# Kernel optimization log

Measured on AMD Instinct MI355X. Metric: run time of the kernel, lower is better.

## Reference

```python
import jax, jax.numpy as jnp
import numpy as np

NUM_EXPERTS = 8
TOP_K = 2
HIDDEN = 2048
FFN = 4096


def setup_inputs() -> dict:
    key = jax.random.key(0)
    ks = jax.random.split(key, 5)
    s = 0.02
    return {
        "hidden_states": jax.random.normal(ks[0], (2, 2048, HIDDEN), dtype=jnp.float32),
        "w_router": jax.random.normal(ks[1], (HIDDEN, NUM_EXPERTS), dtype=jnp.float32) * s,
        "w1": jax.random.normal(ks[2], (NUM_EXPERTS, FFN, HIDDEN), dtype=jnp.float32) * s,
        "w2": jax.random.normal(ks[3], (NUM_EXPERTS, HIDDEN, FFN), dtype=jnp.float32) * s,
        "w3": jax.random.normal(ks[4], (NUM_EXPERTS, FFN, HIDDEN), dtype=jnp.float32) * s,
    }


def reference(hidden_states, w_router, w1, w2, w3):
    shape = hidden_states.shape
    x = hidden_states.reshape(-1, HIDDEN)  # [T, H]

    # Router: logits -> softmax -> top-k -> renormalize (Mixtral routing)
    logits = x @ w_router                              # [T, E]
    probs = jax.nn.softmax(logits, axis=-1)
    top_w, top_i = jax.lax.top_k(probs, TOP_K)         # [T, K]
    top_w = top_w / jnp.sum(top_w, axis=-1, keepdims=True)
    # Dense combine weights per expert: [T, E]
    combine = jnp.sum(
        jax.nn.one_hot(top_i, NUM_EXPERTS, dtype=x.dtype) * top_w[..., None], axis=1
    )

    # Grouped SwiGLU experts: out = sum_e combine[:, e] * w2_e(silu(w1_e x) * w3_e x)
    out = jnp.zeros_like(x)
    for e in range(NUM_EXPERTS):
        h = jax.nn.silu(x @ w1[e].T) * (x @ w3[e].T)   # [T, F]
        y = h @ w2[e].T                                # [T, H]
        out = out + combine[:, e:e + 1] * y

    return (out.reshape(shape), jnp.zeros((1,), dtype=x.dtype))
```

## Files before the change

kernel.cpp:

```cpp
#include <hip/hip_runtime.h>
#include <hip/hip_bf16.h>
#include <stdint.h>

#define T_TOK 4096
#define HID   2048
#define FFN_D 4096
#define NE    8
#define PADB  256
#define PADMAX 10240

typedef __attribute__((ext_vector_type(8))) short  short8;
typedef __attribute__((ext_vector_type(4))) float  f32x4;
typedef __attribute__((ext_vector_type(4))) unsigned short u16x4;
typedef unsigned short u16;

__device__ __forceinline__ u16 f2bf(float f) {
    unsigned u = __float_as_uint(f);
    u += 0x7FFFu + ((u >> 16) & 1u);
    return (u16)(u >> 16);
}
__device__ __forceinline__ float bf2f(u16 v) {
    return __uint_as_float(((unsigned)v) << 16);
}

#define GLD16(g, l) __builtin_amdgcn_global_load_lds( \
    (const __attribute__((address_space(1))) unsigned int*)(g), \
    (__attribute__((address_space(3))) unsigned int*)(l), 16, 0, 0)

__global__ void k_convert(const float* __restrict__ s, u16* __restrict__ d, long n8) {
    for (long i = (long)blockIdx.x * 256 + threadIdx.x; i < n8; i += (long)gridDim.x * 256) {
        f32x4 a = *((const f32x4*)s + i * 2);
        f32x4 b = *((const f32x4*)s + i * 2 + 1);
        short8 o;
#pragma unroll
        for (int q = 0; q < 4; ++q) { o[q] = (short)f2bf(a[q]); o[q + 4] = (short)f2bf(b[q]); }
        *(short8*)(d + i * 8) = o;
    }
}

__global__ void k_router(const float* __restrict__ x, const float* __restrict__ wr,
                         int* __restrict__ topk_id, float* __restrict__ topk_w,
                         int* __restrict__ counts) {
    int lane = threadIdx.x & 63;
    int t = blockIdx.x * 4 + (threadIdx.x >> 6);
    const float* xr = x + (size_t)t * HID;
    float acc[8];
#pragma unroll
    for (int e = 0; e < 8; ++e) acc[e] = 0.f;
    for (int h = lane; h < HID; h += 64) {
        float xv = xr[h];
        f32x4 w0 = *(const f32x4*)(wr + h * 8);
        f32x4 w1 = *(const f32x4*)(wr + h * 8 + 4);
#pragma unroll
        for (int q = 0; q < 4; ++q) { acc[q] += xv * w0[q]; acc[4 + q] += xv * w1[q]; }
    }
#pragma unroll
    for (int e = 0; e < 8; ++e) {
        float v = acc[e];
#pragma unroll
        for (int s = 32; s > 0; s >>= 1) v += __shfl_xor(v, s);
        acc[e] = v;
    }
    if (lane == 0) {
        int i0 = 0; float l0 = acc[0];
#pragma unroll
        for (int e = 1; e < 8; ++e) if (acc[e] > l0) { l0 = acc[e]; i0 = e; }
        int i1 = -1; float l1 = -3.4e38f;
#pragma unroll
        for (int e = 0; e < 8; ++e) if (e != i0 && acc[e] > l1) { l1 = acc[e]; i1 = e; }
        float wA = 1.f / (1.f + expf(l1 - l0));
        topk_id[t * 2] = i0;  topk_id[t * 2 + 1] = i1;
        topk_w[t * 2] = wA;   topk_w[t * 2 + 1] = 1.f - wA;
        atomicAdd(&counts[i0], 1);
        atomicAdd(&counts[i1], 1);
    }
}

__global__ void k_scan(const int* __restrict__ counts, int* __restrict__ pad_off,
                       int* __restrict__ perm_tok) {
    __shared__ int sTot;
    if (threadIdx.x == 0) {
        int o = 0;
#pragma unroll
        for (int e = 0; e < 8; ++e) { pad_off[e] = o; o += ((counts[e] + PADB - 1) / PADB) * PADB; }
        pad_off[8] = o; sTot = o;
    }
    __syncthreads();
    int tot = sTot;
    for (int i = threadIdx.x; i < tot; i += 256) perm_tok[i] = 0;
}

__global__ void k_scatter(const int* __restrict__ topk_id, int* __restrict__ cursors,
                          const int* __restrict__ pad_off, int* __restrict__ perm_tok,
                          int* __restrict__ pos_of) {
    int t = blockIdx.x * 256 + threadIdx.x;
    if (t >= T_TOK) return;
#pragma unroll
    for (int k = 0; k < 2; ++k) {
        int e = topk_id[t * 2 + k];
        int p = pad_off[e] + atomicAdd(&cursors[e], 1);
        perm_tok[p] = t;
        pos_of[t * 2 + k] = p;
    }
}

template<int KTOT, int NTOT, int BNt, int KSPLIT, bool DUAL, bool GATHER>
__global__ __launch_bounds__(512, 2) void k_gemm8(
    const u16* __restrict__ A,
    const u16* __restrict__ B0all,
    const u16* __restrict__ B1all,
    u16* __restrict__ C,
    const int* __restrict__ perm_tok,
    const int* __restrict__ pad_off)
{
    constexpr int BMt   = 256;
    constexpr int WCW   = BNt / 4;
    constexpr int NI    = WCW / 16;
    constexpr int CPX   = (NTOT / BNt) / 8;
    constexpr int KPART = KTOT / KSPLIT;
    constexpr int NK    = KPART / 64;
    constexpr int ATILE = BMt * 64;
    constexpr int BTILE = BNt * 64;
    constexpr int SEGB  = DUAL ? 8 : (BNt == 256 ? 8 : 4);

    const int bid = blockIdx.x;
    const int xcd = bid & 7;
    int idx = bid >> 3;
    const int kh  = idx & (KSPLIT - 1);
    idx /= KSPLIT;
    const int m0  = (idx / CPX) * BMt;
    if (m0 >= pad_off[8]) return;
    const int n0  = (xcd * CPX + (idx % CPX)) * BNt;
    int e = 0;
    while (pad_off[e + 1] <= m0) ++e;

    __shared__ u16 As[2 * ATILE];
    __shared__ u16 Bs0[2 * BTILE];
    __shared__ u16 Bs1[DUAL ? 2 * BTILE : 8];
    __shared__ int tokS[GATHER ? BMt : 8];

    const int tid = threadIdx.x;
    const int w = tid >> 6, l = tid & 63;
    if (GATHER) {
        for (int i = tid; i < BMt; i += 512) tokS[i] = perm_tok[m0 + i];
        __syncthreads();
    }

    const u16* B0 = B0all + (size_t)e * NTOT * KTOT;
    const u16* B1 = DUAL ? (B1all + (size_t)e * NTOT * KTOT) : B0all;
    const int k0e = kh * KPART;

    const int nseg = (w < 4) ? 8 : SEGB;
    const u16* gsrc[8];
    u16* ldst[8];
    int tstep;
    {
        const int c = (l & 7) ^ (l >> 3);
#pragma unroll
        for (int j = 0; j < 8; ++j) {
            const int js = (j < nseg) ? j : (j - 4);
            const int rl = js * 8 + (l >> 3);
            if (w < 4) {
                const int rt = w * 64 + rl;
                const long grow = GATHER ? (long)tokS[rt] : (long)(m0 + rt);
                gsrc[j] = A + grow * KTOT + k0e + c * 8;
                ldst[j] = (u16*)As + (w * 64 + js * 8) * 64;
                tstep = ATILE;
            } else if (DUAL && w >= 6) {
                const int rt = (w - 6) * 64 + rl;
                gsrc[j] = B1 + (size_t)(n0 + rt) * KTOT + k0e + c * 8;
                ldst[j] = (u16*)Bs1 + (rt - rl + js * 8) * 64;
                tstep = BTILE;
            } else {
                const int rt = DUAL ? ((w - 4) * 64 + rl)
                                    : (BNt == 256 ? ((w - 4) * 64 + rl)
                                                  : ((w - 4) * 32 + rl));
                gsrc[j] = B0 + (size_t)(n0 + rt) * KTOT + k0e + c * 8;
                ldst[j] = (u16*)Bs0 + (rt - rl + js * 8) * 64;
                tstep = BTILE;
            }
        }
    }

    const int wr = w >> 2, wc = w & 3;
    const int fr = l & 15, fk = l >> 4, x7 = l & 7;
    const int pc0 = ((fk ^ x7) << 3);
    const int pc1 = pc0 ^ 32;
    const int aB = (wr * 128 + fr) * 64;
    const int bB = (wc * WCW + fr) * 64;

    f32x4 acc0[8][NI], acc1[8][NI];
    const f32x4 fz = {0.f, 0.f, 0.f, 0.f};
#pragma unroll
    for (int mi = 0; mi < 8; ++mi)
#pragma unroll
        for (int ni = 0; ni < NI; ++ni) { acc0[mi][ni] = fz; if (DUAL) acc1[mi][ni] = fz; }

#pragma unroll
    for (int j = 0; j < 8; ++j) if (j < nseg) GLD16(gsrc[j], ldst[j]);
    asm volatile("s_waitcnt vmcnt(0)" ::: "memory");
    __builtin_amdgcn_s_barrier();
    __builtin_amdgcn_sched_barrier(0);

#pragma unroll 1
    for (int t = 0; t < NK; ++t) {
        const int cb = t & 1, nb2 = cb ^ 1;
        const u16* aC  = (const u16*)As  + cb * ATILE;
        const u16* b0C = (const u16*)Bs0 + cb * BTILE;
        const u16* b1C = (const u16*)Bs1 + (DUAL ? cb * BTILE : 0);
        const long kE = (long)(t + 1) * 64;
        const bool hasNext = (t + 1 < NK);

        short8 af[4], b0f[NI], b1f[NI];

        if (hasNext) {
#pragma unroll
            for (int j = 0; j < 4; ++j) if (j < nseg) GLD16(gsrc[j] + kE, ldst[j] + nb2 * tstep);
        }
#pragma unroll
        for (int mi = 0; mi < 4; ++mi) af[mi] = *(const short8*)(aC + aB + mi * 1024 + pc0);
#pragma unroll
        for (int ni = 0; ni < NI; ++ni) {
            b0f[ni] = *(const short8*)(b0C + bB + ni * 1024 + pc0);
            if (DUAL) b1f[ni] = *(const short8*)(b1C + bB + ni * 1024 + pc0);
        }
        __builtin_amdgcn_s_setprio(1);
#pragma unroll
        for (int mi = 0; mi < 4; ++mi)
#pragma unroll
            for (int ni = 0; ni < NI; ++ni) {
                acc0[mi][ni] = __builtin_amdgcn_mfma_f32_16x16x32_bf16(af[mi], b0f[ni], acc0[mi][ni], 0, 0, 0);
                if (DUAL)
                    acc1[mi][ni] = __builtin_amdgcn_mfma_f32_16x16x32_bf16(af[mi], b1f[ni], acc1[mi][ni], 0, 0, 0);
            }
        __builtin_amdgcn_s_setprio(0);

        if (hasNext) {
#pragma unroll
            for (int j = 4; j < 8; ++j) if (j < nseg) GLD16(gsrc[j] + kE, ldst[j] + nb2 * tstep);
        }
#pragma unroll
        for (int mi = 0; mi < 4; ++mi) af[mi] = *(const short8*)(aC + aB + (mi + 4) * 1024 + pc0);
        __builtin_amdgcn_s_setprio(1);
#pragma unroll
        for (int mi = 0; mi < 4; ++mi)
#pragma unroll
            for (int ni = 0; ni < NI; ++ni) {
                acc0[mi + 4][ni] = __builtin_amdgcn_mfma_f32_16x16x32_bf16(af[mi], b0f[ni], acc0[mi + 4][ni], 0, 0, 0);
                if (DUAL)
                    acc1[mi + 4][ni] = __builtin_amdgcn_mfma_f32_16x16x32_bf16(af[mi], b1f[ni], acc1[mi + 4][ni], 0, 0, 0);
            }
        __builtin_amdgcn_s_setprio(0);

#pragma unroll
        for (int mi = 0; mi < 4; ++mi) af[mi] = *(const short8*)(aC + aB + mi * 1024 + pc1);
#pragma unroll
        for (int ni = 0; ni < NI; ++ni) {
            b0f[ni] = *(const short8*)(b0C + bB + ni * 1024 + pc1);
            if (DUAL) b1f[ni] = *(const short8*)(b1C + bB + ni * 1024 + pc1);
        }
        __builtin_amdgcn_s_setprio(1);
#pragma unroll
        for (int mi = 0; mi < 4; ++mi)
#pragma unroll
            for (int ni = 0; ni < NI; ++ni) {
                acc0[mi][ni] = __builtin_amdgcn_mfma_f32_16x16x32_bf16(af[mi], b0f[ni], acc0[mi][ni], 0, 0, 0);
                if (DUAL)
                    acc1[mi][ni] = __builtin_amdgcn_mfma_f32_16x16x32_bf16(af[mi], b1f[ni], acc1[mi][ni], 0, 0, 0);
            }
        __builtin_amdgcn_s_setprio(0);

#pragma unroll
        for (int mi = 0; mi < 4; ++mi) af[mi] = *(const short8*)(aC + aB + (mi + 4) * 1024 + pc1);
        __builtin_amdgcn_s_setprio(1);
#pragma unroll
        for (int mi = 0; mi < 4; ++mi)
#pragma unroll
            for (int ni = 0; ni < NI; ++ni) {
                acc0[mi + 4][ni] = __builtin_amdgcn_mfma_f32_16x16x32_bf16(af[mi], b0f[ni], acc0[mi + 4][ni], 0, 0, 0);
                if (DUAL)
                    acc1[mi + 4][ni] = __builtin_amdgcn_mfma_f32_16x16x32_bf16(af[mi], b1f[ni], acc1[mi + 4][ni], 0, 0, 0);
            }
        __builtin_amdgcn_s_setprio(0);

        asm volatile("s_waitcnt vmcnt(0)" ::: "memory");
        __builtin_amdgcn_s_barrier();
        __builtin_amdgcn_sched_barrier(0);
    }

    u16* Co = C + (KSPLIT > 1 ? (size_t)kh * PADMAX * NTOT : 0);
    const int er = (l >> 4) * 4;
    const int ec = l & 15;
#pragma unroll
    for (int mi = 0; mi < 8; ++mi)
#pragma unroll
        for (int ni = 0; ni < NI; ++ni)
#pragma unroll
            for (int r = 0; r < 4; ++r) {
                size_t prow = (size_t)(m0 + wr * 128 + mi * 16 + er + r);
                int col = n0 + wc * WCW + ni * 16 + ec;
                float v = acc0[mi][ni][r];
                float res;
                if (DUAL) {
                    float g3 = acc1[mi][ni][r];
                    res = v / (1.f + __expf(-v)) * g3;
                } else {
                    res = v;
                }
                Co[prow * NTOT + col] = f2bf(res);
            }
}

__global__ void k_combine2(const u16* __restrict__ y0, const u16* __restrict__ y1,
                           const int* __restrict__ pos_of,
                           const float* __restrict__ topk_w, float* __restrict__ out) {
    int idx = blockIdx.x * 256 + threadIdx.x;
    int t  = idx >> 9;
    int c4 = (idx & 511) << 2;
    int p0 = pos_of[t * 2], p1 = pos_of[t * 2 + 1];
    float w0 = topk_w[t * 2], w1 = topk_w[t * 2 + 1];
    u16x4 a0 = *(const u16x4*)(y0 + (size_t)p0 * HID + c4);
    u16x4 a1 = *(const u16x4*)(y1 + (size_t)p0 * HID + c4);
    u16x4 b0 = *(const u16x4*)(y0 + (size_t)p1 * HID + c4);
    u16x4 b1 = *(const u16x4*)(y1 + (size_t)p1 * HID + c4);
    f32x4 o;
#pragma unroll
    for (int q = 0; q < 4; ++q)
        o[q] = w0 * (bf2f(a0[q]) + bf2f(a1[q])) + w1 * (bf2f(b0[q]) + bf2f(b1[q]));
    *(f32x4*)(out + (size_t)t * HID + c4) = o;
    if (idx == 0) out[(size_t)T_TOK * HID] = 0.f;
}

__global__ void k_init(int* __restrict__ c) {
    if (threadIdx.x < 16) c[threadIdx.x] = 0;
}

extern "C" void kernel_launch(void* const* d_in, const int* in_sizes, int n_in,
                              void* d_out, int out_size, void* d_ws, size_t ws_size,
                              hipStream_t stream) {
    const float* x  = (const float*)d_in[0];
    const float* wr = (const float*)d_in[1];
    const float* w1 = (const float*)d_in[2];
    const float* w2 = (const float*)d_in[3];
    const float* w3 = (const float*)d_in[4];
    float* out = (float*)d_out;
    char* ws = (char*)d_ws;

    u16*  xb  = (u16*)(ws);
    u16*  wA  = (u16*)(ws + 16777216);
    u16*  w3b = (u16*)(ws + 150994944);
    u16*  hb  = (u16*)(ws + 285212672);
    u16*  yb  = (u16*)(ws + 150994944);
    int*  perm_tok = (int*)(ws + 369098752);
    int*  pos_of   = (int*)(ws + 369139712);
    int*  topk_id  = (int*)(ws + 369172480);
    float* topk_w  = (float*)(ws + 369205248);
    int*  cnt      = (int*)(ws + 369238016);
    int*  counts   = cnt;
    int*  cursors  = cnt + 8;
    int*  pad_off  = cnt + 16;

    k_init<<<1, 64, 0, stream>>>(cnt);
    k_convert<<<2048, 256, 0, stream>>>(x, xb, (long)T_TOK * HID / 8);
    k_router<<<1024, 256, 0, stream>>>(x, wr, topk_id, topk_w, counts);
    k_scan<<<1, 256, 0, stream>>>(counts, pad_off, perm_tok);
    k_scatter<<<16, 256, 0, stream>>>(topk_id, cursors, pad_off, perm_tok, pos_of);

    const long WN8 = (long)NE * FFN_D * HID / 8;
    k_convert<<<4096, 256, 0, stream>>>(w1, wA, WN8);
    k_convert<<<4096, 256, 0, stream>>>(w3, w3b, WN8);

    k_gemm8<HID, FFN_D, 128, 1, true, true><<<(FFN_D / 128) * 40, 512, 0, stream>>>(
        xb, wA, w3b, hb, perm_tok, pad_off);

    k_convert<<<4096, 256, 0, stream>>>(w2, wA, WN8);

    k_gemm8<FFN_D, HID, 256, 2, false, false><<<(HID / 256) * 40 * 2, 512, 0, stream>>>(
        hb, wA, (const u16*)nullptr, yb, perm_tok, pad_off);

    k_combine2<<<8192, 256, 0, stream>>>(yb, yb + (size_t)PADMAX * HID,
                                         pos_of, topk_w, out);
}
```

Before: 869.8 us.

## Fuse x conversion into router, merge w1/w3 converts, overlap w2 convert with GEMM1

The router kernel now also writes the bf16 copy of x, so one full read of x and one launch go away. The w1 and w3 fp32-to-bf16 conversions are merged into a single launch. When the workspace is large enough, the w2 conversion runs in 512 extra blocks appended to the first grouped GEMM, writing into a separate buffer so it overlaps with GEMM work instead of running as its own serial pass. This needs a larger workspace, and the conversion blocks compete with GEMM blocks for CUs and memory bandwidth.

```diff
diff --git a/kernel.cpp b/kernel.cpp
--- a/kernel.cpp
+++ b/kernel.cpp
@@ -38,17 +38,35 @@
     }
 }
 
+__global__ void k_convert2(const float* __restrict__ s0, u16* __restrict__ d0,
+                           const float* __restrict__ s1, u16* __restrict__ d1, long n8) {
+    for (long i = (long)blockIdx.x * 256 + threadIdx.x; i < 2 * n8; i += (long)gridDim.x * 256) {
+        const float* s = (i < n8) ? s0 : s1;
+        u16*         d = (i < n8) ? d0 : d1;
+        long         j = (i < n8) ? i : (i - n8);
+        f32x4 a = *((const f32x4*)s + j * 2);
+        f32x4 b = *((const f32x4*)s + j * 2 + 1);
+        short8 o;
+#pragma unroll
+        for (int q = 0; q < 4; ++q) { o[q] = (short)f2bf(a[q]); o[q + 4] = (short)f2bf(b[q]); }
+        *(short8*)(d + j * 8) = o;
+    }
+}
+
 __global__ void k_router(const float* __restrict__ x, const float* __restrict__ wr,
+                         u16* __restrict__ xb,
                          int* __restrict__ topk_id, float* __restrict__ topk_w,
                          int* __restrict__ counts) {
     int lane = threadIdx.x & 63;
     int t = blockIdx.x * 4 + (threadIdx.x >> 6);
     const float* xr = x + (size_t)t * HID;
+    u16* xbr = xb + (size_t)t * HID;
     float acc[8];
 #pragma unroll
     for (int e = 0; e < 8; ++e) acc[e] = 0.f;
     for (int h = lane; h < HID; h += 64) {
         float xv = xr[h];
+        xbr[h] = f2bf(xv);
         f32x4 w0 = *(const f32x4*)(wr + h * 8);
         f32x4 w1 = *(const f32x4*)(wr + h * 8 + 4);
 #pragma unroll
@@ -104,14 +122,17 @@
     }
 }
 
-template<int KTOT, int NTOT, int BNt, int KSPLIT, bool DUAL, bool GATHER>
+template<int KTOT, int NTOT, int BNt, int KSPLIT, bool DUAL, bool GATHER, bool CONV>
 __global__ __launch_bounds__(512, 2) void k_gemm8(
     const u16* __restrict__ A,
     const u16* __restrict__ B0all,
     const u16* __restrict__ B1all,
     u16* __restrict__ C,
     const int* __restrict__ perm_tok,
-    const int* __restrict__ pad_off)
+    const int* __restrict__ pad_off,
+    const float* __restrict__ W2c,
+    u16* __restrict__ W2d,
+    int gemmBlk, int convBlk)
 {
     constexpr int BMt   = 256;
     constexpr int WCW   = BNt / 4;
@@ -124,6 +145,22 @@
     constexpr int SEGB  = DUAL ? 8 : (BNt == 256 ? 8 : 4);
 
     const int bid = blockIdx.x;
+    const int tid = threadIdx.x;
+
+    if (CONV && bid >= gemmBlk) {
+        const long per = (long)NE * FFN_D * HID / 8 / convBlk;
+        const long i0 = (long)(bid - gemmBlk) * per;
+        for (long i = i0 + tid; i < i0 + per; i += 512) {
+            f32x4 a = *((const f32x4*)W2c + i * 2);
+            f32x4 b = *((const f32x4*)W2c + i * 2 + 1);
+            short8 o;
+#pragma unroll
+            for (int q = 0; q < 4; ++q) { o[q] = (short)f2bf(a[q]); o[q + 4] = (short)f2bf(b[q]); }
+            *(short8*)(W2d + i * 8) = o;
+        }
+        return;
+    }
+
     const int xcd = bid & 7;
     int idx = bid >> 3;
     const int kh  = idx & (KSPLIT - 1);
@@ -139,7 +176,6 @@
     __shared__ u16 Bs1[DUAL ? 2 * BTILE : 8];
     __shared__ int tokS[GATHER ? BMt : 8];
 
-    const int tid = threadIdx.x;
     const int w = tid >> 6, l = tid & 63;
     if (GATHER) {
         for (int i = tid; i < BMt; i += 512) tokS[i] = perm_tok[m0 + i];
@@ -346,38 +382,78 @@
     float* out = (float*)d_out;
     char* ws = (char*)d_ws;
 
-    u16*  xb  = (u16*)(ws);
-    u16*  wA  = (u16*)(ws + 16777216);
-    u16*  w3b = (u16*)(ws + 150994944);
-    u16*  hb  = (u16*)(ws + 285212672);
-    u16*  yb  = (u16*)(ws + 150994944);
-    int*  perm_tok = (int*)(ws + 369098752);
-    int*  pos_of   = (int*)(ws + 369139712);
-    int*  topk_id  = (int*)(ws + 369172480);
-    float* topk_w  = (float*)(ws + 369205248);
-    int*  cnt      = (int*)(ws + 369238016);
-    int*  counts   = cnt;
-    int*  cursors  = cnt + 8;
-    int*  pad_off  = cnt + 16;
-
-    k_init<<<1, 64, 0, stream>>>(cnt);
-    k_convert<<<2048, 256, 0, stream>>>(x, xb, (long)T_TOK * HID / 8);
-    k_router<<<1024, 256, 0, stream>>>(x, wr, topk_id, topk_w, counts);
-    k_scan<<<1, 256, 0, stream>>>(counts, pad_off, perm_tok);
-    k_scatter<<<16, 256, 0, stream>>>(topk_id, cursors, pad_off, perm_tok, pos_of);
-
     const long WN8 = (long)NE * FFN_D * HID / 8;
-    k_convert<<<4096, 256, 0, stream>>>(w1, wA, WN8);
-    k_convert<<<4096, 256, 0, stream>>>(w3, w3b, WN8);
-
-    k_gemm8<HID, FFN_D, 128, 1, true, true><<<(FFN_D / 128) * 40, 512, 0, stream>>>(
-        xb, wA, w3b, hb, perm_tok, pad_off);
-
-    k_convert<<<4096, 256, 0, stream>>>(w2, wA, WN8);
-
-    k_gemm8<FFN_D, HID, 256, 2, false, false><<<(HID / 256) * 40 * 2, 512, 0, stream>>>(
-        hb, wA, (const u16*)nullptr, yb, perm_tok, pad_off);
-
-    k_combine2<<<8192, 256, 0, stream>>>(yb, yb + (size_t)PADMAX * HID,
-                                         pos_of, topk_w, out);
-}
+    const size_t NEED = 503459840ull;
+
+    if (ws_size >= NEED) {
+        u16*  xb  = (u16*)(ws);
+        u16*  wA  = (u16*)(ws + 16777216);
+        u16*  w3b = (u16*)(ws + 150994944);
+        u16*  hb  = (u16*)(ws + 285212672);
+        u16*  w2b = (u16*)(ws + 369098752);
+        u16*  yb  = (u16*)(ws + 150994944);
+        int*  perm_tok = (int*)(ws + 503316480);
+        int*  pos_of   = (int*)(ws + 503357440);
+        int*  topk_id  = (int*)(ws + 503390208);
+        float* topk_w  = (float*)(ws + 503422976);
+        int*  cnt      = (int*)(ws + 503455744);
+        int*  counts   = cnt;
+        int*  cursors  = cnt + 8;
+        int*  pad_off  = cnt + 16;
+
+        k_init<<<1, 64, 0, stream>>>(cnt);
+        k_router<<<1024, 256, 0, stream>>>(x, wr, xb, topk_id, topk_w, counts);
+        k_scan<<<1, 256, 0, stream>>>(counts, pad_off, perm_tok);
+        k_scatter<<<16, 256, 0, stream>>>(topk_id, cursors, pad_off, perm_tok, pos_of);
+
+        k_convert2<<<8192, 256, 0, stream>>>(w1, wA, w3, w3b, WN8);
+
+        k_gemm8<HID, FFN_D, 128, 1, true, true, true>
+            <<<(FFN_D / 128) * 40 + 512, 512, 0, stream>>>(
+            xb, wA, w3b, hb, perm_tok, pad_off, w2, w2b, (FFN_D / 128) * 40, 512);
+
+        k_gemm8<FFN_D, HID, 256, 2, false, false, false>
+            <<<(HID / 256) * 40 * 2, 512, 0, stream>>>(
+            hb, w2b, (const u16*)nullptr, yb, perm_tok, pad_off,
+            (const float*)nullptr, (u16*)nullptr, 0, 0);
+
+        k_combine2<<<8192, 256, 0, stream>>>(yb, yb + (size_t)PADMAX * HID,
+                                             pos_of, topk_w, out);
+    } else {
+        u16*  xb  = (u16*)(ws);
+        u16*  wA  = (u16*)(ws + 16777216);
+        u16*  w3b = (u16*)(ws + 150994944);
+        u16*  hb  = (u16*)(ws + 285212672);
+        u16*  yb  = (u16*)(ws + 150994944);
+        int*  perm_tok = (int*)(ws + 369098752);
+        int*  pos_of   = (int*)(ws + 369139712);
+        int*  topk_id  = (int*)(ws + 369172480);
+        float* topk_w  = (float*)(ws + 369205248);
+        int*  cnt      = (int*)(ws + 369238016);
+        int*  counts   = cnt;
+        int*  cursors  = cnt + 8;
+        int*  pad_off  = cnt + 16;
+
+        k_init<<<1, 64, 0, stream>>>(cnt);
+        k_router<<<1024, 256, 0, stream>>>(x, wr, xb, topk_id, topk_w, counts);
+        k_scan<<<1, 256, 0, stream>>>(counts, pad_off, perm_tok);
+        k_scatter<<<16, 256, 0, stream>>>(topk_id, cursors, pad_off, perm_tok, pos_of);
+
+        k_convert2<<<8192, 256, 0, stream>>>(w1, wA, w3, w3b, WN8);
+
+        k_gemm8<HID, FFN_D, 128, 1, true, true, false>
+            <<<(FFN_D / 128) * 40, 512, 0, stream>>>(
+            xb, wA, w3b, hb, perm_tok, pad_off,
+            (const float*)nullptr, (u16*)nullptr, 0, 0);
+
+        k_convert<<<4096, 256, 0, stream>>>(w2, wA, WN8);
+
+        k_gemm8<FFN_D, HID, 256, 2, false, false, false>
+            <<<(HID / 256) * 40 * 2, 512, 0, stream>>>(
+            hb, wA, (const u16*)nullptr, yb, perm_tok, pad_off,
+            (const float*)nullptr, (u16*)nullptr, 0, 0);
+
+        k_combine2<<<8192, 256, 0, stream>>>(yb, yb + (size_t)PADMAX * HID,
+                                             pos_of, topk_w, out);
+    }
+}
```

Result: no change. 853.1 us (-1.9%).
